# Kernel tuning notes

Hardware: AMD Instinct MI355X
Metric: run time of the kernel (lower is better)

Reference implementation:

```python
import jax, jax.numpy as jnp
import numpy as np

# Module hyperparameters (from init_kwargs)
NBITS = 8
FOLD = 8
B = 8192
IN_F = 2048
OUT_F = 2048
ISIZE = IN_F // FOLD   # 256
OSIZE = OUT_F // FOLD  # 256
QMAX = 2 ** (NBITS - 1) - 1  # 127


def setup_inputs() -> dict:
    key = jax.random.key(0)
    k1, k2, k3, k4, k5 = jax.random.split(key, 5)
    inp = jax.random.normal(k1, (B, IN_F), dtype=jnp.float32)
    # per-fold linear weights, torch nn.Linear default-ish scale
    W = jax.random.normal(k2, (FOLD, OSIZE, ISIZE), dtype=jnp.float32) * (1.0 / np.sqrt(ISIZE))
    # UniformPositionalEncoding buffers: offset + per-fold per-column ranges
    pe = jax.random.normal(k3, (1, FOLD, ISIZE), dtype=jnp.float32) * 0.1
    min_range = -jax.random.uniform(k4, (1, FOLD, ISIZE), minval=0.25, maxval=1.0, dtype=jnp.float32)
    max_range = jax.random.uniform(k5, (1, FOLD, ISIZE), minval=0.25, maxval=1.0, dtype=jnp.float32)
    return {"input": inp, "W": W, "pe": pe, "min_range": min_range, "max_range": max_range}


def reference(input, W, pe, min_range, max_range):
    b = input.shape[0]
    x = input.reshape(b, FOLD, ISIZE)
    # QuantAct symmetric, clamp_only=True: per-tensor scale s = max|x| / n, clamp to [-s*n, s*n]
    s = jnp.max(jnp.abs(x)) / QMAX
    x = jnp.clip(x, -s * QMAX, s * QMAX)
    s = s * QMAX  # scaled range multiplier
    # positional offset, broadcast over batch
    x = x + pe[0]  # [b, FOLD, ISIZE]
    x_flat = x.reshape(b * FOLD, ISIZE)

    def per_fold(Wi, mn, mx):
        # fold_idx_ste forward passes full x through; range mask zeroes out-of-range entries
        mask = (x_flat < mn * s) | (x_flat > mx * s)  # [b*FOLD, ISIZE]
        xm = jnp.where(mask, jnp.float32(0.0), x_flat)
        o = xm @ Wi.T  # [b*FOLD, OSIZE]
        return o.reshape(b, FOLD, OSIZE).sum(axis=1)  # [b, OSIZE]

    # vmap over the FOLD small linears
    out = jax.vmap(per_fold)(W, min_range[0], max_range[0])  # [FOLD, b, OSIZE]
    out = jnp.transpose(out, (1, 0, 2)).reshape(b, FOLD * OSIZE)  # stack dim=1 then flatten
    return out
```

## Files before the change

kernel.cpp:

```cpp
#include <hip/hip_runtime.h>

#define FOLD  8
#define ISIZE 256
#define IN_F  2048
#define OUT_F 2048
#define TBM   32
#define NBLK  (8192 / TBM)
#define CHW   1104

typedef __attribute__((ext_vector_type(8))) short short8;
typedef __attribute__((ext_vector_type(4))) float f32x4;

__device__ __forceinline__ unsigned f2bf(float f) {
    unsigned u = __float_as_uint(f);
    u += 0x7FFFu + ((u >> 16) & 1u);
    return (u >> 16);
}

__global__ __launch_bounds__(256)
void absmax_kernel(const float4* __restrict__ in,
                   float* __restrict__ partials,
                   unsigned int* __restrict__ scal,
                   int quota, int mode) {
    const int nthreads = gridDim.x * 256;
    const int idx = blockIdx.x * 256 + threadIdx.x;
    float m = 0.f;
    #pragma unroll 4
    for (int q = 0; q < quota; ++q) {
        float4 a = in[idx + q * nthreads];
        m = fmaxf(m, fmaxf(fmaxf(fabsf(a.x), fabsf(a.y)),
                           fmaxf(fabsf(a.z), fabsf(a.w))));
    }
    #pragma unroll
    for (int off = 32; off > 0; off >>= 1)
        m = fmaxf(m, __shfl_down(m, off, 64));
    __shared__ float sm[4];
    int lane = threadIdx.x & 63, wv = threadIdx.x >> 6;
    if (lane == 0) sm[wv] = m;
    __syncthreads();
    if (threadIdx.x == 0) {
        float r = fmaxf(fmaxf(sm[0], sm[1]), fmaxf(sm[2], sm[3]));
        if (mode) partials[blockIdx.x] = r;
        else      atomicMax(scal, __float_as_uint(r));
    }
}

__global__ void convert_w_kernel(const float* __restrict__ W,
                                 unsigned short* __restrict__ wsw) {
    int t    = blockIdx.x * 256 + threadIdx.x;
    int wid  = t >> 6;
    int lane = t & 63;
    int i  = wid >> 7;
    int nt = (wid >> 3) & 15;
    int ks = wid & 7;
    int n = lane & 15, q = lane >> 4;
    const float* src = W + (((size_t)i * 256 + nt * 16 + n) * 256 + ks * 32 + q * 8);
    float4 s0 = *(const float4*)(src);
    float4 s1 = *(const float4*)(src + 4);
    uint4 p;
    p.x = f2bf(s0.x) | (f2bf(s0.y) << 16);
    p.y = f2bf(s0.z) | (f2bf(s0.w) << 16);
    p.z = f2bf(s1.x) | (f2bf(s1.y) << 16);
    p.w = f2bf(s1.z) | (f2bf(s1.w) << 16);
    *(uint4*)(wsw + (size_t)wid * 512 + lane * 8) = p;
}

template<int PRECONV>
__global__ __launch_bounds__(1024, 1)
void fold_main(const float* __restrict__ in,
               const float* __restrict__ W,
               const unsigned short* __restrict__ wsw,
               const float* __restrict__ pe,
               const float* __restrict__ mn,
               const float* __restrict__ mx,
               const float* __restrict__ partials,
               const unsigned int* __restrict__ scal,
               int npart,
               float* __restrict__ out) {
    __shared__ __align__(16) unsigned short ylds[64 * CHW];
    __shared__ float sred[16];

    const int tid  = threadIdx.x;
    const int lane = tid & 63;
    const int wv   = tid >> 6;
    const int row0 = blockIdx.x * TBM;

    float mabs;
    if (npart > 0) {
        float v = (tid < npart) ? partials[tid] : 0.0f;
        #pragma unroll
        for (int off = 32; off > 0; off >>= 1)
            v = fmaxf(v, __shfl_down(v, off, 64));
        if (lane == 0) sred[wv] = v;
        __syncthreads();
        float r = sred[0];
        #pragma unroll
        for (int i = 1; i < 16; ++i) r = fmaxf(r, sred[i]);
        mabs = r;
    } else {
        mabs = __uint_as_float(*scal);
    }
    const float c = (mabs / 127.0f) * 127.0f;

    {
        const int kp  = tid & 127;
        const int rq  = tid >> 7;
        const int k0  = kp * 2;
        const int jh  = kp & 3;
        const int qA  = (kp >> 2) & 3;
        const int ksA = kp >> 4;

        float pef[FOLD][2], lo[FOLD][2], hi[FOLD][2];
        #pragma unroll
        for (int f = 0; f < FOLD; ++f) {
            float2 p2 = *(const float2*)(pe + f * ISIZE + k0);
            pef[f][0] = p2.x; pef[f][1] = p2.y;
        }
        #pragma unroll
        for (int i = 0; i < FOLD; ++i) {
            float2 a2 = *(const float2*)(mn + i * ISIZE + k0);
            float2 b2 = *(const float2*)(mx + i * ISIZE + k0);
            lo[i][0] = a2.x * c; lo[i][1] = a2.y * c;
            hi[i][0] = b2.x * c; hi[i][1] = b2.y * c;
        }

        #pragma unroll
        for (int r4 = 0; r4 < 4; ++r4) {
            const int row = rq * 4 + r4;
            const float* rowp = in + (size_t)(row0 + row) * IN_F + k0;
            float2 xr[FOLD];
            #pragma unroll
            for (int f = 0; f < FOLD; ++f) xr[f] = *(const float2*)(rowp + f * ISIZE);

            float acc[FOLD][2];
            #pragma unroll
            for (int i = 0; i < FOLD; ++i) { acc[i][0] = 0.0f; acc[i][1] = 0.0f; }
            #pragma unroll
            for (int f = 0; f < FOLD; ++f) {
                float xv0 = fminf(fmaxf(xr[f].x, -c), c) + pef[f][0];
                float xv1 = fminf(fmaxf(xr[f].y, -c), c) + pef[f][1];
                #pragma unroll
                for (int i = 0; i < FOLD; ++i) {
                    if (xv0 >= lo[i][0] && xv0 <= hi[i][0]) acc[i][0] += xv0;
                    if (xv1 >= lo[i][1] && xv1 <= hi[i][1]) acc[i][1] += xv1;
                }
            }
            const unsigned base = (unsigned)((row >> 4) * 544 + qA * 136 + (row & 15) * 8 + jh * 2);
            #pragma unroll
            for (int i = 0; i < FOLD; ++i) {
                unsigned us = f2bf(acc[i][0]) | (f2bf(acc[i][1]) << 16);
                *(unsigned*)&ylds[(i * 8 + ksA) * CHW + base] = us;
            }
        }
    }
    __syncthreads();

    {
        const int fi   = wv >> 1;
        const int nh   = wv & 1;
        const int mrow = lane & 15;
        const int quad = lane >> 4;

        short8 afr[8][2];
        #pragma unroll
        for (int kk = 0; kk < 8; ++kk) {
            #pragma unroll
            for (int mt = 0; mt < 2; ++mt)
                afr[kk][mt] = *(const short8*)&ylds[(fi * 8 + kk) * CHW + mt * 544 + quad * 136 + mrow * 8];
        }

        const int col0 = fi * 256 + mrow;
        #pragma unroll 2
        for (int nt8 = 0; nt8 < 8; ++nt8) {
            const int ntg = nh * 8 + nt8;
            f32x4 a0 = (f32x4){0.f, 0.f, 0.f, 0.f};
            f32x4 a1 = (f32x4){0.f, 0.f, 0.f, 0.f};
            if (PRECONV) {
                const unsigned short* wb = wsw + ((size_t)(fi * 16 + ntg) * 8) * 512 + lane * 8;
                uint4 wq[8];
                #pragma unroll
                for (int kk = 0; kk < 8; ++kk) wq[kk] = *(const uint4*)(wb + kk * 512);
                #pragma unroll
                for (int kk = 0; kk < 8; ++kk) {
                    union { uint4 u; short8 s; } cv; cv.u = wq[kk];
                    a0 = __builtin_amdgcn_mfma_f32_16x16x32_bf16(afr[kk][0], cv.s, a0, 0, 0, 0);
                    a1 = __builtin_amdgcn_mfma_f32_16x16x32_bf16(afr[kk][1], cv.s, a1, 0, 0, 0);
                }
            } else {
                const float* wb = W + ((size_t)(fi * 256 + ntg * 16 + mrow) * 256 + quad * 8);
                float4 w[16];
                #pragma unroll
                for (int kk = 0; kk < 8; ++kk) {
                    w[2 * kk]     = *(const float4*)(wb + kk * 32);
                    w[2 * kk + 1] = *(const float4*)(wb + kk * 32 + 4);
                }
                #pragma unroll
                for (int kk = 0; kk < 8; ++kk) {
                    union { uint4 u; short8 s; } cv;
                    cv.u.x = f2bf(w[2*kk].x)   | (f2bf(w[2*kk].y)   << 16);
                    cv.u.y = f2bf(w[2*kk].z)   | (f2bf(w[2*kk].w)   << 16);
                    cv.u.z = f2bf(w[2*kk+1].x) | (f2bf(w[2*kk+1].y) << 16);
                    cv.u.w = f2bf(w[2*kk+1].z) | (f2bf(w[2*kk+1].w) << 16);
                    a0 = __builtin_amdgcn_mfma_f32_16x16x32_bf16(afr[kk][0], cv.s, a0, 0, 0, 0);
                    a1 = __builtin_amdgcn_mfma_f32_16x16x32_bf16(afr[kk][1], cv.s, a1, 0, 0, 0);
                }
            }
            #pragma unroll
            for (int rg = 0; rg < 4; ++rg) {
                out[(size_t)(row0 +      quad * 4 + rg) * OUT_F + col0 + ntg * 16] = a0[rg];
                out[(size_t)(row0 + 16 + quad * 4 + rg) * OUT_F + col0 + ntg * 16] = a1[rg];
            }
        }
    }
}

extern "C" void kernel_launch(void* const* d_in, const int* in_sizes, int n_in,
                              void* d_out, int out_size, void* d_ws, size_t ws_size,
                              hipStream_t stream) {
    const float* in = (const float*)d_in[0];
    const float* W  = (const float*)d_in[1];
    const float* pe = (const float*)d_in[2];
    const float* mn = (const float*)d_in[3];
    const float* mx = (const float*)d_in[4];
    float* out = (float*)d_out;

    const size_t PART_OFF  = 16;
    const size_t WSW_OFF   = 8192;
    const size_t WSW_BYTES = (size_t)FOLD * 256 * 256 * 2;

    unsigned int*   scal     = (unsigned int*)d_ws;
    float*          partials = (float*)((char*)d_ws + PART_OFF);
    unsigned short* wsw      = (unsigned short*)((char*)d_ws + WSW_OFF);

    const bool preconv = ws_size >= WSW_OFF + WSW_BYTES;

    int npart;
    if (ws_size >= PART_OFF + 1024 * sizeof(float)) {
        absmax_kernel<<<1024, 256, 0, stream>>>((const float4*)in, partials, scal, 16, 1);
        npart = 1024;
    } else if (ws_size >= PART_OFF + 256 * sizeof(float)) {
        absmax_kernel<<<256, 256, 0, stream>>>((const float4*)in, partials, scal, 64, 1);
        npart = 256;
    } else {
        hipMemsetAsync(d_ws, 0, sizeof(unsigned int), stream);
        absmax_kernel<<<256, 256, 0, stream>>>((const float4*)in, partials, scal, 64, 0);
        npart = 0;
    }

    if (preconv) {
        convert_w_kernel<<<256, 256, 0, stream>>>(W, wsw);
        fold_main<1><<<NBLK, 1024, 0, stream>>>(in, W, wsw, pe, mn, mx,
                                                partials, scal, npart, out);
    } else {
        fold_main<0><<<NBLK, 1024, 0, stream>>>(in, W, wsw, pe, mn, mx,
                                                partials, scal, npart, out);
    }
}
```

Baseline: 153.3 us.

## Fuse absmax, weight conversion and fold GEMM into one grid-barrier kernel

Replaces the three launches (absmax reduction, weight bf16 conversion, main fold kernel) with a single persistent kernel. Each block computes the absmax of its own 32 rows, the first 64 blocks convert W to bf16, and all blocks then meet at an atomic-counter spin barrier before running the fold body. This removes launch gaps and the separate full pass over the input, and the block's rows are likely still in cache for the main phase. The barrier relies on all 256 blocks being co-resident, which is plausible on a 256-CU part with one block per CU but is not guaranteed, and it adds a memset plus spin latency.

```diff
diff --git a/kernel.cpp b/kernel.cpp
--- a/kernel.cpp
+++ b/kernel.cpp
@@ -65,6 +65,200 @@
     *(uint4*)(wsw + (size_t)wid * 512 + lane * 8) = p;
 }
 
+__device__ __forceinline__ void fold_body(const float* __restrict__ in,
+                                          const unsigned short* __restrict__ wsw,
+                                          const float* __restrict__ pe,
+                                          const float* __restrict__ mn,
+                                          const float* __restrict__ mx,
+                                          float c, int row0,
+                                          unsigned short* ylds,
+                                          float* __restrict__ out) {
+    const int tid  = threadIdx.x;
+    const int lane = tid & 63;
+    const int wv   = tid >> 6;
+
+    {
+        const int kp  = tid & 127;
+        const int rq  = tid >> 7;
+        const int k0  = kp * 2;
+        const int jh  = kp & 3;
+        const int qA  = (kp >> 2) & 3;
+        const int ksA = kp >> 4;
+
+        float pef[FOLD][2], lo[FOLD][2], hi[FOLD][2];
+        #pragma unroll
+        for (int f = 0; f < FOLD; ++f) {
+            float2 p2 = *(const float2*)(pe + f * ISIZE + k0);
+            pef[f][0] = p2.x; pef[f][1] = p2.y;
+        }
+        #pragma unroll
+        for (int i = 0; i < FOLD; ++i) {
+            float2 a2 = *(const float2*)(mn + i * ISIZE + k0);
+            float2 b2 = *(const float2*)(mx + i * ISIZE + k0);
+            lo[i][0] = a2.x * c; lo[i][1] = a2.y * c;
+            hi[i][0] = b2.x * c; hi[i][1] = b2.y * c;
+        }
+
+        #pragma unroll
+        for (int r4 = 0; r4 < 4; ++r4) {
+            const int row = rq * 4 + r4;
+            const float* rowp = in + (size_t)(row0 + row) * IN_F + k0;
+            float2 xr[FOLD];
+            #pragma unroll
+            for (int f = 0; f < FOLD; ++f) xr[f] = *(const float2*)(rowp + f * ISIZE);
+
+            float acc[FOLD][2];
+            #pragma unroll
+            for (int i = 0; i < FOLD; ++i) { acc[i][0] = 0.0f; acc[i][1] = 0.0f; }
+            #pragma unroll
+            for (int f = 0; f < FOLD; ++f) {
+                float xv0 = fminf(fmaxf(xr[f].x, -c), c) + pef[f][0];
+                float xv1 = fminf(fmaxf(xr[f].y, -c), c) + pef[f][1];
+                #pragma unroll
+                for (int i = 0; i < FOLD; ++i) {
+                    if (xv0 >= lo[i][0] && xv0 <= hi[i][0]) acc[i][0] += xv0;
+                    if (xv1 >= lo[i][1] && xv1 <= hi[i][1]) acc[i][1] += xv1;
+                }
+            }
+            const unsigned base = (unsigned)((row >> 4) * 544 + qA * 136 + (row & 15) * 8 + jh * 2);
+            #pragma unroll
+            for (int i = 0; i < FOLD; ++i) {
+                unsigned us = f2bf(acc[i][0]) | (f2bf(acc[i][1]) << 16);
+                *(unsigned*)&ylds[(i * 8 + ksA) * CHW + base] = us;
+            }
+        }
+    }
+    __syncthreads();
+
+    {
+        const int fi   = wv >> 1;
+        const int nh   = wv & 1;
+        const int mrow = lane & 15;
+        const int quad = lane >> 4;
+
+        short8 afr[8][2];
+        #pragma unroll
+        for (int kk = 0; kk < 8; ++kk) {
+            #pragma unroll
+            for (int mt = 0; mt < 2; ++mt)
+                afr[kk][mt] = *(const short8*)&ylds[(fi * 8 + kk) * CHW + mt * 544 + quad * 136 + mrow * 8];
+        }
+
+        const int col0 = fi * 256 + mrow;
+        #pragma unroll 2
+        for (int nt8 = 0; nt8 < 8; ++nt8) {
+            const int ntg = nh * 8 + nt8;
+            f32x4 a0 = (f32x4){0.f, 0.f, 0.f, 0.f};
+            f32x4 a1 = (f32x4){0.f, 0.f, 0.f, 0.f};
+            const unsigned short* wb = wsw + ((size_t)(fi * 16 + ntg) * 8) * 512 + lane * 8;
+            uint4 wq[8];
+            #pragma unroll
+            for (int kk = 0; kk < 8; ++kk) wq[kk] = *(const uint4*)(wb + kk * 512);
+            #pragma unroll
+            for (int kk = 0; kk < 8; ++kk) {
+                union { uint4 u; short8 s; } cv; cv.u = wq[kk];
+                a0 = __builtin_amdgcn_mfma_f32_16x16x32_bf16(afr[kk][0], cv.s, a0, 0, 0, 0);
+                a1 = __builtin_amdgcn_mfma_f32_16x16x32_bf16(afr[kk][1], cv.s, a1, 0, 0, 0);
+            }
+            #pragma unroll
+            for (int rg = 0; rg < 4; ++rg) {
+                out[(size_t)(row0 +      quad * 4 + rg) * OUT_F + col0 + ntg * 16] = a0[rg];
+                out[(size_t)(row0 + 16 + quad * 4 + rg) * OUT_F + col0 + ntg * 16] = a1[rg];
+            }
+        }
+    }
+}
+
+__global__ __launch_bounds__(1024, 1)
+void fused_spin(const float* __restrict__ in,
+                const float* __restrict__ W,
+                unsigned short* __restrict__ wsw,
+                const float* __restrict__ pe,
+                const float* __restrict__ mn,
+                const float* __restrict__ mx,
+                unsigned int* __restrict__ counter,
+                float* __restrict__ partials,
+                float* __restrict__ out) {
+    __shared__ __align__(16) unsigned short ylds[64 * CHW];
+    __shared__ float sred[16];
+
+    const int tid  = threadIdx.x;
+    const int lane = tid & 63;
+    const int wv   = tid >> 6;
+    const int row0 = blockIdx.x * TBM;
+
+    {
+        const float4* in4 = (const float4*)(in + (size_t)row0 * IN_F);
+        float m = 0.f;
+        #pragma unroll 4
+        for (int q = 0; q < 16; ++q) {
+            float4 a = in4[tid + q * 1024];
+            m = fmaxf(m, fmaxf(fmaxf(fabsf(a.x), fabsf(a.y)),
+                               fmaxf(fabsf(a.z), fabsf(a.w))));
+        }
+        #pragma unroll
+        for (int off = 32; off > 0; off >>= 1)
+            m = fmaxf(m, __shfl_down(m, off, 64));
+        if (lane == 0) sred[wv] = m;
+    }
+
+    if (blockIdx.x < 64) {
+        const int g    = blockIdx.x * 1024 + tid;
+        const int wid  = g >> 6;
+        const int l    = g & 63;
+        const int i  = wid >> 7;
+        const int nt = (wid >> 3) & 15;
+        const int ks = wid & 7;
+        const int n = l & 15, q = l >> 4;
+        const float* src = W + (((size_t)i * 256 + nt * 16 + n) * 256 + ks * 32 + q * 8);
+        float4 s0 = *(const float4*)(src);
+        float4 s1 = *(const float4*)(src + 4);
+        unsigned long long w0 = (unsigned long long)(f2bf(s0.x) | (f2bf(s0.y) << 16))
+                              | ((unsigned long long)(f2bf(s0.z) | (f2bf(s0.w) << 16)) << 32);
+        unsigned long long w1 = (unsigned long long)(f2bf(s1.x) | (f2bf(s1.y) << 16))
+                              | ((unsigned long long)(f2bf(s1.z) | (f2bf(s1.w) << 16)) << 32);
+        unsigned long long* dst = (unsigned long long*)(wsw + (size_t)wid * 512 + l * 8);
+        __hip_atomic_store(&dst[0], w0, __ATOMIC_RELAXED, __HIP_MEMORY_SCOPE_AGENT);
+        __hip_atomic_store(&dst[1], w1, __ATOMIC_RELAXED, __HIP_MEMORY_SCOPE_AGENT);
+    }
+
+    __syncthreads();
+
+    if (tid == 0) {
+        float r = sred[0];
+        #pragma unroll
+        for (int i = 1; i < 16; ++i) r = fmaxf(r, sred[i]);
+        __hip_atomic_store(&partials[blockIdx.x], r, __ATOMIC_RELAXED, __HIP_MEMORY_SCOPE_AGENT);
+        __threadfence();
+        __hip_atomic_fetch_add(counter, 1u, __ATOMIC_RELEASE, __HIP_MEMORY_SCOPE_AGENT);
+        for (int it = 0; it < (1 << 20); ++it) {
+            unsigned v = __hip_atomic_load(counter, __ATOMIC_ACQUIRE, __HIP_MEMORY_SCOPE_AGENT);
+            if (v >= NBLK) break;
+            __builtin_amdgcn_s_sleep(1);
+        }
+    }
+    __syncthreads();
+
+    float mabs;
+    {
+        float v = (tid < NBLK)
+            ? __hip_atomic_load(&partials[tid], __ATOMIC_RELAXED, __HIP_MEMORY_SCOPE_AGENT)
+            : 0.0f;
+        #pragma unroll
+        for (int off = 32; off > 0; off >>= 1)
+            v = fmaxf(v, __shfl_down(v, off, 64));
+        if (lane == 0) sred[wv] = v;
+        __syncthreads();
+        float r = sred[0];
+        #pragma unroll
+        for (int i = 1; i < 16; ++i) r = fmaxf(r, sred[i]);
+        mabs = r;
+    }
+    const float c = (mabs / 127.0f) * 127.0f;
+
+    fold_body(in, wsw, pe, mn, mx, c, row0, ylds, out);
+}
+
 template<int PRECONV>
 __global__ __launch_bounds__(1024, 1)
 void fold_main(const float* __restrict__ in,
@@ -102,91 +296,82 @@
     }
     const float c = (mabs / 127.0f) * 127.0f;
 
-    {
-        const int kp  = tid & 127;
-        const int rq  = tid >> 7;
-        const int k0  = kp * 2;
-        const int jh  = kp & 3;
-        const int qA  = (kp >> 2) & 3;
-        const int ksA = kp >> 4;
-
-        float pef[FOLD][2], lo[FOLD][2], hi[FOLD][2];
-        #pragma unroll
-        for (int f = 0; f < FOLD; ++f) {
-            float2 p2 = *(const float2*)(pe + f * ISIZE + k0);
-            pef[f][0] = p2.x; pef[f][1] = p2.y;
-        }
-        #pragma unroll
-        for (int i = 0; i < FOLD; ++i) {
-            float2 a2 = *(const float2*)(mn + i * ISIZE + k0);
-            float2 b2 = *(const float2*)(mx + i * ISIZE + k0);
-            lo[i][0] = a2.x * c; lo[i][1] = a2.y * c;
-            hi[i][0] = b2.x * c; hi[i][1] = b2.y * c;
-        }
-
-        #pragma unroll
-        for (int r4 = 0; r4 < 4; ++r4) {
-            const int row = rq * 4 + r4;
-            const float* rowp = in + (size_t)(row0 + row) * IN_F + k0;
-            float2 xr[FOLD];
-            #pragma unroll
-            for (int f = 0; f < FOLD; ++f) xr[f] = *(const float2*)(rowp + f * ISIZE);
-
-            float acc[FOLD][2];
-            #pragma unroll
-            for (int i = 0; i < FOLD; ++i) { acc[i][0] = 0.0f; acc[i][1] = 0.0f; }
+    if (PRECONV) {
+        fold_body(in, wsw, pe, mn, mx, c, row0, ylds, out);
+    } else {
+        {
+            const int kp  = tid & 127;
+            const int rq  = tid >> 7;
+            const int k0  = kp * 2;
+            const int jh  = kp & 3;
+            const int qA  = (kp >> 2) & 3;
+            const int ksA = kp >> 4;
+
+            float pef[FOLD][2], lo[FOLD][2], hi[FOLD][2];
             #pragma unroll
             for (int f = 0; f < FOLD; ++f) {
-                float xv0 = fminf(fmaxf(xr[f].x, -c), c) + pef[f][0];
-                float xv1 = fminf(fmaxf(xr[f].y, -c), c) + pef[f][1];
+                float2 p2 = *(const float2*)(pe + f * ISIZE + k0);
+                pef[f][0] = p2.x; pef[f][1] = p2.y;
+            }
+            #pragma unroll
+            for (int i = 0; i < FOLD; ++i) {
+                float2 a2 = *(const float2*)(mn + i * ISIZE + k0);
+                float2 b2 = *(const float2*)(mx + i * ISIZE + k0);
+                lo[i][0] = a2.x * c; lo[i][1] = a2.y * c;
+                hi[i][0] = b2.x * c; hi[i][1] = b2.y * c;
+            }
+
+            #pragma unroll
+            for (int r4 = 0; r4 < 4; ++r4) {
+                const int row = rq * 4 + r4;
+                const float* rowp = in + (size_t)(row0 + row) * IN_F + k0;
+                float2 xr[FOLD];
+                #pragma unroll
+                for (int f = 0; f < FOLD; ++f) xr[f] = *(const float2*)(rowp + f * ISIZE);
+
+                float acc[FOLD][2];
+                #pragma unroll
+                for (int i = 0; i < FOLD; ++i) { acc[i][0] = 0.0f; acc[i][1] = 0.0f; }
+                #pragma unroll
+                for (int f = 0; f < FOLD; ++f) {
+                    float xv0 = fminf(fmaxf(xr[f].x, -c), c) + pef[f][0];
+                    float xv1 = fminf(fmaxf(xr[f].y, -c), c) + pef[f][1];
+                    #pragma unroll
+                    for (int i = 0; i < FOLD; ++i) {
+                        if (xv0 >= lo[i][0] && xv0 <= hi[i][0]) acc[i][0] += xv0;
+                        if (xv1 >= lo[i][1] && xv1 <= hi[i][1]) acc[i][1] += xv1;
+                    }
+                }
+                const unsigned base = (unsigned)((row >> 4) * 544 + qA * 136 + (row & 15) * 8 + jh * 2);
                 #pragma unroll
                 for (int i = 0; i < FOLD; ++i) {
-                    if (xv0 >= lo[i][0] && xv0 <= hi[i][0]) acc[i][0] += xv0;
-                    if (xv1 >= lo[i][1] && xv1 <= hi[i][1]) acc[i][1] += xv1;
-                }
-            }
-            const unsigned base = (unsigned)((row >> 4) * 544 + qA * 136 + (row & 15) * 8 + jh * 2);
-            #pragma unroll
-            for (int i = 0; i < FOLD; ++i) {
-                unsigned us = f2bf(acc[i][0]) | (f2bf(acc[i][1]) << 16);
-                *(unsigned*)&ylds[(i * 8 + ksA) * CHW + base] = us;
-            }
-        }
-    }
-    __syncthreads();
-
-    {
-        const int fi   = wv >> 1;
-        const int nh   = wv & 1;
-        const int mrow = lane & 15;
-        const int quad = lane >> 4;
-
-        short8 afr[8][2];
-        #pragma unroll
-        for (int kk = 0; kk < 8; ++kk) {
-            #pragma unroll
-            for (int mt = 0; mt < 2; ++mt)
-                afr[kk][mt] = *(const short8*)&ylds[(fi * 8 + kk) * CHW + mt * 544 + quad * 136 + mrow * 8];
-        }
-
-        const int col0 = fi * 256 + mrow;
-        #pragma unroll 2
-        for (int nt8 = 0; nt8 < 8; ++nt8) {
-            const int ntg = nh * 8 + nt8;
-            f32x4 a0 = (f32x4){0.f, 0.f, 0.f, 0.f};
-            f32x4 a1 = (f32x4){0.f, 0.f, 0.f, 0.f};
-            if (PRECONV) {
-                const unsigned short* wb = wsw + ((size_t)(fi * 16 + ntg) * 8) * 512 + lane * 8;
-                uint4 wq[8];
-                #pragma unroll
-                for (int kk = 0; kk < 8; ++kk) wq[kk] = *(const uint4*)(wb + kk * 512);
-                #pragma unroll
-                for (int kk = 0; kk < 8; ++kk) {
-                    union { uint4 u; short8 s; } cv; cv.u = wq[kk];
-                    a0 = __builtin_amdgcn_mfma_f32_16x16x32_bf16(afr[kk][0], cv.s, a0, 0, 0, 0);
-                    a1 = __builtin_amdgcn_mfma_f32_16x16x32_bf16(afr[kk][1], cv.s, a1, 0, 0, 0);
-                }
-            } else {
+                    unsigned us = f2bf(acc[i][0]) | (f2bf(acc[i][1]) << 16);
+                    *(unsigned*)&ylds[(i * 8 + ksA) * CHW + base] = us;
+                }
+            }
+        }
+        __syncthreads();
+
+        {
+            const int fi   = wv >> 1;
+            const int nh   = wv & 1;
+            const int mrow = lane & 15;
+            const int quad = lane >> 4;
+
+            short8 afr[8][2];
+            #pragma unroll
+            for (int kk = 0; kk < 8; ++kk) {
+                #pragma unroll
+                for (int mt = 0; mt < 2; ++mt)
+                    afr[kk][mt] = *(const short8*)&ylds[(fi * 8 + kk) * CHW + mt * 544 + quad * 136 + mrow * 8];
+            }
+
+            const int col0 = fi * 256 + mrow;
+            #pragma unroll 2
+            for (int nt8 = 0; nt8 < 8; ++nt8) {
+                const int ntg = nh * 8 + nt8;
+                f32x4 a0 = (f32x4){0.f, 0.f, 0.f, 0.f};
+                f32x4 a1 = (f32x4){0.f, 0.f, 0.f, 0.f};
                 const float* wb = W + ((size_t)(fi * 256 + ntg * 16 + mrow) * 256 + quad * 8);
                 float4 w[16];
                 #pragma unroll
@@ -204,11 +389,11 @@
                     a0 = __builtin_amdgcn_mfma_f32_16x16x32_bf16(afr[kk][0], cv.s, a0, 0, 0, 0);
                     a1 = __builtin_amdgcn_mfma_f32_16x16x32_bf16(afr[kk][1], cv.s, a1, 0, 0, 0);
                 }
-            }
-            #pragma unroll
-            for (int rg = 0; rg < 4; ++rg) {
-                out[(size_t)(row0 +      quad * 4 + rg) * OUT_F + col0 + ntg * 16] = a0[rg];
-                out[(size_t)(row0 + 16 + quad * 4 + rg) * OUT_F + col0 + ntg * 16] = a1[rg];
+                #pragma unroll
+                for (int rg = 0; rg < 4; ++rg) {
+                    out[(size_t)(row0 +      quad * 4 + rg) * OUT_F + col0 + ntg * 16] = a0[rg];
+                    out[(size_t)(row0 + 16 + quad * 4 + rg) * OUT_F + col0 + ntg * 16] = a1[rg];
+                }
             }
         }
     }
@@ -225,14 +410,23 @@
     float* out = (float*)d_out;
 
     const size_t PART_OFF  = 16;
+    const size_t PART2_OFF = 512;
     const size_t WSW_OFF   = 8192;
     const size_t WSW_BYTES = (size_t)FOLD * 256 * 256 * 2;
 
     unsigned int*   scal     = (unsigned int*)d_ws;
     float*          partials = (float*)((char*)d_ws + PART_OFF);
+    float*          part2    = (float*)((char*)d_ws + PART2_OFF);
     unsigned short* wsw      = (unsigned short*)((char*)d_ws + WSW_OFF);
 
     const bool preconv = ws_size >= WSW_OFF + WSW_BYTES;
+
+    if (preconv) {
+        hipMemsetAsync(d_ws, 0, 64, stream);
+        fused_spin<<<NBLK, 1024, 0, stream>>>(in, W, wsw, pe, mn, mx,
+                                              (unsigned int*)d_ws, part2, out);
+        return;
+    }
 
     int npart;
     if (ws_size >= PART_OFF + 1024 * sizeof(float)) {
@@ -246,13 +440,6 @@
         absmax_kernel<<<256, 256, 0, stream>>>((const float4*)in, partials, scal, 64, 0);
         npart = 0;
     }
-
-    if (preconv) {
-        convert_w_kernel<<<256, 256, 0, stream>>>(W, wsw);
-        fold_main<1><<<NBLK, 1024, 0, stream>>>(in, W, wsw, pe, mn, mx,
-                                                partials, scal, npart, out);
-    } else {
-        fold_main<0><<<NBLK, 1024, 0, stream>>>(in, W, wsw, pe, mn, mx,
-                                                partials, scal, npart, out);
-    }
-}
+    fold_main<0><<<NBLK, 1024, 0, stream>>>(in, W, wsw, pe, mn, mx,
+                                            partials, scal, npart, out);
+}
```

After: 189.7 us. +23.7%, slower.
